# Kernel tuning notes

Measured on AMD Instinct MI355X. Metric: run time of the kernel, lower is better.

## Reference

```python
import jax, jax.numpy as jnp
import numpy as np

N_NODES = 50000
N_EDGES = 800000
HIDDEN = 128
IN_DIM = 128
OUT_DIM = 40
N_LAYERS = 3


def setup_inputs() -> dict:
    key = jax.random.key(0)
    ks = jax.random.split(key, 8)
    s = 1.0 / np.sqrt(HIDDEN)
    return {
        "x": jax.random.normal(ks[0], (N_NODES, IN_DIM), jnp.float32),
        "edge_index": jax.random.randint(ks[1], (2, N_EDGES), 0, N_NODES, jnp.int32),
        "W_in": jax.random.normal(ks[2], (IN_DIM, HIDDEN), jnp.float32) * s,
        "b_in": jnp.zeros((HIDDEN,), jnp.float32),
        "Wl": jax.random.normal(ks[3], (N_LAYERS, HIDDEN, HIDDEN), jnp.float32) * s,
        "Wr": jax.random.normal(ks[4], (N_LAYERS, HIDDEN, HIDDEN), jnp.float32) * s,
        "bl": jnp.zeros((N_LAYERS, HIDDEN), jnp.float32),
        "Wc1": jax.random.normal(ks[5], (HIDDEN, HIDDEN), jnp.float32) * s,
        "bc1": jnp.zeros((HIDDEN,), jnp.float32),
        "Wc2": jax.random.normal(ks[6], (HIDDEN, OUT_DIM), jnp.float32) * s,
        "bc2": jnp.zeros((OUT_DIM,), jnp.float32),
    }


def reference(x, edge_index, W_in, b_in, Wl, Wr, bl, Wc1, bc1, Wc2, bc2):
    src, dst = edge_index[0], edge_index[1]
    n = x.shape[0]
    # in-degree for mean aggregation (clamped to 1 for isolated nodes)
    deg = jax.ops.segment_sum(jnp.ones_like(src, x.dtype), dst, num_segments=n)
    deg_inv = (1.0 / jnp.maximum(deg, 1.0))[:, None]  # [N,1]

    h = x @ W_in + b_in  # lin1; dropout is identity in eval mode
    js = []
    for i in range(N_LAYERS):
        # GraphSAGE-mean: gather neighbor feats, scatter-mean, self + neighbor linear
        agg = jax.ops.segment_sum(h[src], dst, num_segments=n) * deg_inv
        h = jax.nn.relu(h @ Wl[i] + agg @ Wr[i] + bl[i])
        js.append(h)  # skip ops are identity; fix_last appends last layer directly

    x5 = js[0] + js[1] + js[2]  # layer aggregator 'l_sum' with linear activation
    hc = jax.nn.relu(x5 @ Wc1 + bc1)
    return hc @ Wc2 + bc2  # logits [N, OUT_DIM]
```

## Files before the change

kernel.cpp:

```cpp
#include <hip/hip_runtime.h>
#include <hip/hip_fp8.h>

#define NN   50000
#define NE   800000
#define HID  128
#define OUTD 40
#define NBLK 196
#define LIN_BLKS ((NN + 127) / 128)
#define DEG_BLKS ((NE + 255) / 256)

typedef float f32x4  __attribute__((ext_vector_type(4)));
typedef int   i32x4  __attribute__((ext_vector_type(4)));
typedef short bf16x8 __attribute__((ext_vector_type(8)));

__device__ __forceinline__ f32x4 mfma(bf16x8 a, bf16x8 b, f32x4 c) {
  return __builtin_amdgcn_mfma_f32_16x16x32_bf16(a, b, c, 0, 0, 0);
}
__device__ __forceinline__ unsigned short f2bf(float f) {
  unsigned u = __builtin_bit_cast(unsigned, f);
  u += 0x7fffu + ((u >> 16) & 1u);
  return (unsigned short)(u >> 16);
}
__device__ __forceinline__ unsigned pack2(float lo, float hi) {
  return (unsigned)f2bf(lo) | ((unsigned)f2bf(hi) << 16);
}
__device__ __forceinline__ float bflo(unsigned v){ return __builtin_bit_cast(float, v << 16); }
__device__ __forceinline__ float bfhi(unsigned v){ return __builtin_bit_cast(float, v & 0xffff0000u); }
__device__ __forceinline__ unsigned char f2fp8(float f) {
  return (unsigned char)__hip_fp8_e4m3(f).__x;
}
__device__ __forceinline__ void accfp8(float* a, uint4 v) {
  unsigned u[4] = {v.x, v.y, v.z, v.w};
#pragma unroll
  for (int i = 0; i < 4; i++) {
#pragma unroll
    for (int b = 0; b < 4; b++) {
      __hip_fp8_e4m3 t;
      t.__x = (__hip_fp8_storage_t)((u[i] >> (8 * b)) & 0xffu);
      a[i * 4 + b] += (float)t;
    }
  }
}

__global__ void k_blocksum(const int* __restrict__ deg, int* __restrict__ bsum) {
  __shared__ int s[256];
  int t = threadIdx.x, i = blockIdx.x * 256 + t;
  s[t] = (i < NN) ? deg[i] : 0;
  __syncthreads();
  for (int o = 128; o > 0; o >>= 1) { if (t < o) s[t] += s[t + o]; __syncthreads(); }
  if (t == 0) bsum[blockIdx.x] = s[0];
}

__global__ void k_scan3(const int* __restrict__ deg, const int* __restrict__ bsum,
                        int* __restrict__ offs, float* __restrict__ dinv) {
  __shared__ int sb[256];
  __shared__ int s[256];
  int t = threadIdx.x, i = blockIdx.x * 256 + t;
  sb[t] = (t < NBLK && t < blockIdx.x) ? bsum[t] : 0;
  int v = (i < NN) ? deg[i] : 0;
  s[t] = v;
  __syncthreads();
  for (int o = 128; o > 0; o >>= 1) { if (t < o) sb[t] += sb[t + o]; __syncthreads(); }
  for (int o = 1; o < 256; o <<= 1) {
    int x = (t >= o) ? s[t - o] : 0;
    __syncthreads(); s[t] += x; __syncthreads();
  }
  int off = sb[0] + s[t] - v;
  if (i < NN) {
    offs[i] = off;
    dinv[i] = 1.0f / (float)(v > 0 ? v : 1);
  }
  if (i == 0) offs[NN] = NE;
}

__global__ void k_fill(const int* __restrict__ src, const int* __restrict__ dst,
                       const int* __restrict__ pos, const int* __restrict__ offs,
                       int* __restrict__ csr) {
  int i = blockIdx.x * blockDim.x + threadIdx.x;
  if (i < NE) {
    csr[offs[dst[i]] + pos[i]] = src[i];
  }
}

__global__ void k_prep(const float* __restrict__ Win, const float* __restrict__ Wl,
                       const float* __restrict__ Wr, const float* __restrict__ Wc1,
                       const float* __restrict__ Wc2, unsigned short* __restrict__ wt,
                       int* __restrict__ deg) {
  int idx = blockIdx.x * 256 + threadIdx.x;
  if (idx < NN) deg[idx] = 0;
  const int NMAIN = 8 * 16384;
  if (idx >= NMAIN + 48 * 128) return;
  float v;
  if (idx < NMAIN) {
    int m = idx >> 14, rem = idx & 16383;
    int n = rem >> 7, k = rem & 127;
    const float* s;
    if (m == 0) s = Win;
    else if (m <= 3) s = Wl + (m - 1) * 16384;
    else if (m <= 6) s = Wr + (m - 4) * 16384;
    else s = Wc1;
    v = s[k * 128 + n];
  } else {
    int rem = idx - NMAIN;
    int n = rem >> 7, k = rem & 127;
    v = (n < OUTD) ? Wc2[k * OUTD + n] : 0.f;
  }
  wt[idx] = f2bf(v);
}

__device__ __forceinline__ void lin_in_body(int bid, const float* __restrict__ x,
                                            const unsigned short* __restrict__ Wt,
                                            const float* __restrict__ bias,
                                            unsigned short* __restrict__ hout,
                                            unsigned char* __restrict__ h8out) {
  const int lane = threadIdx.x & 63, w = threadIdx.x >> 6;
  const int wr = w >> 1, wc = w & 1;
  const int r15 = lane & 15, khi = lane >> 4;
  const int mbase = bid * 128 + wr * 64, nbase = wc * 64;
  f32x4 acc[4][4] = {};
#pragma unroll
  for (int ks = 0; ks < 4; ++ks) {
    const int kk = ks * 32 + khi * 8;
    bf16x8 af[4], bq[4];
#pragma unroll
    for (int i = 0; i < 4; i++) {
      int row = mbase + i * 16 + r15; row = row < NN ? row : NN - 1;
      const f32x4* p = (const f32x4*)(x + row * HID + kk);
      f32x4 lo = p[0], hi = p[1];
      i32x4 t;
      t[0] = pack2(lo[0], lo[1]); t[1] = pack2(lo[2], lo[3]);
      t[2] = pack2(hi[0], hi[1]); t[3] = pack2(hi[2], hi[3]);
      af[i] = __builtin_bit_cast(bf16x8, t);
    }
#pragma unroll
    for (int j = 0; j < 4; j++) {
      int col = nbase + j * 16 + r15;
      bq[j] = *(const bf16x8*)(Wt + col * HID + kk);
    }
#pragma unroll
    for (int i = 0; i < 4; i++)
#pragma unroll
      for (int j = 0; j < 4; j++) acc[i][j] = mfma(af[i], bq[j], acc[i][j]);
  }
  float b4[4];
#pragma unroll
  for (int j = 0; j < 4; j++) b4[j] = bias[nbase + j * 16 + r15];
#pragma unroll
  for (int i = 0; i < 4; i++) {
    const int rb = mbase + i * 16 + khi * 4;
#pragma unroll
    for (int e = 0; e < 4; e++) {
      const int r = rb + e;
      if (r < NN) {
#pragma unroll
        for (int j = 0; j < 4; j++) {
          float v = acc[i][j][e] + b4[j];
          const int col = nbase + j * 16 + r15;
          hout[r * HID + col] = f2bf(v);
          h8out[r * HID + col] = f2fp8(v);
        }
      }
    }
  }
}

__global__ __launch_bounds__(256) void k_deg_lin(const int* __restrict__ dst,
                                                 int* __restrict__ deg,
                                                 int* __restrict__ pos,
                                                 const float* __restrict__ x,
                                                 const unsigned short* __restrict__ Wt,
                                                 const float* __restrict__ bias,
                                                 unsigned short* __restrict__ hout,
                                                 unsigned char* __restrict__ h8out) {
  if (blockIdx.x < LIN_BLKS) {
    lin_in_body(blockIdx.x, x, Wt, bias, hout, h8out);
  } else {
    int i = (blockIdx.x - LIN_BLKS) * 256 + threadIdx.x;
    if (i < NE) pos[i] = atomicAdd(&deg[dst[i]], 1);
  }
}

__global__ __launch_bounds__(256) void k_agg(const unsigned char* __restrict__ h8,
                                             const int* __restrict__ csr,
                                             const int* __restrict__ offs,
                                             const float* __restrict__ dinv,
                                             unsigned short* __restrict__ agg) {
  const int lane = threadIdx.x & 63;
  const int c8 = lane & 7;
  const int o8 = lane >> 3;
  int gw = (blockIdx.x * 256 + (int)threadIdx.x) >> 6;
  const int nw = (gridDim.x * 256) >> 6;
  const uint4* h4 = (const uint4*)h8;
  uint4* ag4 = (uint4*)agg;
  for (int n = gw; n < NN; n += nw) {
    const int s = offs[n], e = offs[n + 1];
    float a[16];
#pragma unroll
    for (int j = 0; j < 16; j++) a[j] = 0.f;
    int k = s;
    int ia = 0, ib = 0;
    bool have = (k + 16 <= e);
    if (have) { ia = csr[k + o8]; ib = csr[k + 8 + o8]; }
    while (have) {
      uint4 va = h4[ia * 8 + c8];
      uint4 vb = h4[ib * 8 + c8];
      k += 16;
      have = (k + 16 <= e);
      if (have) { ia = csr[k + o8]; ib = csr[k + 8 + o8]; }
      accfp8(a, va);
      accfp8(a, vb);
    }
    for (; k < e; k += 8) {
      if (k + o8 < e) {
        uint4 v = h4[csr[k + o8] * 8 + c8];
        accfp8(a, v);
      }
    }
#pragma unroll
    for (int j = 0; j < 16; j++) {
      a[j] += __shfl_xor(a[j], 8);
      a[j] += __shfl_xor(a[j], 16);
      a[j] += __shfl_xor(a[j], 32);
    }
    if (o8 == 0) {
      float di = dinv[n];
      uint4 o0, o1;
      o0.x = pack2(a[0] * di, a[1] * di);
      o0.y = pack2(a[2] * di, a[3] * di);
      o0.z = pack2(a[4] * di, a[5] * di);
      o0.w = pack2(a[6] * di, a[7] * di);
      o1.x = pack2(a[8] * di, a[9] * di);
      o1.y = pack2(a[10] * di, a[11] * di);
      o1.z = pack2(a[12] * di, a[13] * di);
      o1.w = pack2(a[14] * di, a[15] * di);
      ag4[n * 16 + c8 * 2 + 0] = o0;
      ag4[n * 16 + c8 * 2 + 1] = o1;
    }
  }
}

__global__ __launch_bounds__(256) void k_layer(const unsigned short* __restrict__ hp,
                                               const unsigned short* __restrict__ ag,
                                               const unsigned short* __restrict__ WtL,
                                               const unsigned short* __restrict__ WtR,
                                               const float* __restrict__ bias,
                                               unsigned short* __restrict__ hout,
                                               unsigned char* __restrict__ h8out) {
  const int lane = threadIdx.x & 63, w = threadIdx.x >> 6;
  const int wr = w >> 1, wc = w & 1;
  const int r15 = lane & 15, khi = lane >> 4;
  const int mbase = blockIdx.x * 128 + wr * 64, nbase = wc * 64;
  f32x4 acc[4][4] = {};
#pragma unroll
  for (int ph = 0; ph < 2; ++ph) {
    const unsigned short* A = ph ? ag : hp;
    const unsigned short* B = ph ? WtR : WtL;
#pragma unroll
    for (int ks = 0; ks < 4; ++ks) {
      const int kk = ks * 32 + khi * 8;
      bf16x8 af[4], bq[4];
#pragma unroll
      for (int i = 0; i < 4; i++) {
        int row = mbase + i * 16 + r15; row = row < NN ? row : NN - 1;
        af[i] = *(const bf16x8*)(A + row * HID + kk);
      }
#pragma unroll
      for (int j = 0; j < 4; j++) {
        int col = nbase + j * 16 + r15;
        bq[j] = *(const bf16x8*)(B + col * HID + kk);
      }
#pragma unroll
      for (int i = 0; i < 4; i++)
#pragma unroll
        for (int j = 0; j < 4; j++) acc[i][j] = mfma(af[i], bq[j], acc[i][j]);
    }
  }
  float b4[4];
#pragma unroll
  for (int j = 0; j < 4; j++) b4[j] = bias[nbase + j * 16 + r15];
#pragma unroll
  for (int i = 0; i < 4; i++) {
    const int rb = mbase + i * 16 + khi * 4;
#pragma unroll
    for (int e = 0; e < 4; e++) {
      const int r = rb + e;
      if (r < NN) {
#pragma unroll
        for (int j = 0; j < 4; j++) {
          float v = acc[i][j][e] + b4[j];
          v = fmaxf(v, 0.f);
          const int col = nbase + j * 16 + r15;
          hout[r * HID + col] = f2bf(v);
          h8out[r * HID + col] = f2fp8(v);
        }
      }
    }
  }
}

__global__ __launch_bounds__(256) void k_cls(const unsigned short* __restrict__ h1,
                                             const unsigned short* __restrict__ h2,
                                             const unsigned short* __restrict__ h3,
                                             const unsigned short* __restrict__ WtC1,
                                             const float* __restrict__ bc1,
                                             const unsigned short* __restrict__ WtC2,
                                             const float* __restrict__ bc2,
                                             float* __restrict__ out) {
  __shared__ unsigned short hc[128 * 136];
  const int lane = threadIdx.x & 63, w = threadIdx.x >> 6;
  const int wr = w >> 1, wc = w & 1;
  const int r15 = lane & 15, khi = lane >> 4;
  const int mbase = blockIdx.x * 128 + wr * 64, nbase = wc * 64;
  {
    f32x4 acc[4][4] = {};
#pragma unroll
    for (int ks = 0; ks < 4; ++ks) {
      const int kk = ks * 32 + khi * 8;
      bf16x8 af[4], bq[4];
#pragma unroll
      for (int i = 0; i < 4; i++) {
        int row = mbase + i * 16 + r15; row = row < NN ? row : NN - 1;
        i32x4 u = *(const i32x4*)(h1 + row * HID + kk);
        i32x4 v = *(const i32x4*)(h2 + row * HID + kk);
        i32x4 q = *(const i32x4*)(h3 + row * HID + kk);
        i32x4 t;
#pragma unroll
        for (int cc = 0; cc < 4; cc++) {
          unsigned uu = u[cc], vv = v[cc], qq = q[cc];
          t[cc] = pack2(bflo(uu) + bflo(vv) + bflo(qq), bfhi(uu) + bfhi(vv) + bfhi(qq));
        }
        af[i] = __builtin_bit_cast(bf16x8, t);
      }
#pragma unroll
      for (int j = 0; j < 4; j++) {
        int col = nbase + j * 16 + r15;
        bq[j] = *(const bf16x8*)(WtC1 + col * HID + kk);
      }
#pragma unroll
      for (int i = 0; i < 4; i++)
#pragma unroll
        for (int j = 0; j < 4; j++) acc[i][j] = mfma(af[i], bq[j], acc[i][j]);
    }
    float b4[4];
#pragma unroll
    for (int j = 0; j < 4; j++) b4[j] = bc1[nbase + j * 16 + r15];
#pragma unroll
    for (int i = 0; i < 4; i++) {
      const int rT = wr * 64 + i * 16 + khi * 4;
#pragma unroll
      for (int e = 0; e < 4; e++) {
#pragma unroll
        for (int j = 0; j < 4; j++) {
          float v = fmaxf(acc[i][j][e] + b4[j], 0.f);
          hc[(rT + e) * 136 + nbase + j * 16 + r15] = f2bf(v);
        }
      }
    }
  }
  __syncthreads();
  {
    f32x4 a2[2][3] = {};
#pragma unroll
    for (int ks = 0; ks < 4; ++ks) {
      const int kk = ks * 32 + khi * 8;
      bf16x8 af[2], bq[3];
#pragma unroll
      for (int i = 0; i < 2; i++) {
        int rT = w * 32 + i * 16 + r15;
        af[i] = *(const bf16x8*)&hc[rT * 136 + kk];
      }
#pragma unroll
      for (int j = 0; j < 3; j++) {
        int col = j * 16 + r15;
        bq[j] = *(const bf16x8*)(WtC2 + col * HID + kk);
      }
#pragma unroll
      for (int i = 0; i < 2; i++)
#pragma unroll
        for (int j = 0; j < 3; j++) a2[i][j] = mfma(af[i], bq[j], a2[i][j]);
    }
#pragma unroll
    for (int j = 0; j < 3; j++) {
      const int col = j * 16 + r15;
      const float b = (col < OUTD) ? bc2[col] : 0.f;
#pragma unroll
      for (int i = 0; i < 2; i++) {
        const int rT = w * 32 + i * 16 + khi * 4;
#pragma unroll
        for (int e = 0; e < 4; e++) {
          const int gr = blockIdx.x * 128 + rT + e;
          if (gr < NN && col < OUTD) out[gr * OUTD + col] = a2[i][j][e] + b;
        }
      }
    }
  }
}

extern "C" void kernel_launch(void* const* d_in, const int* in_sizes, int n_in,
                              void* d_out, int out_size, void* d_ws, size_t ws_size,
                              hipStream_t stream) {
  (void)in_sizes; (void)n_in; (void)out_size; (void)ws_size;
  const float* x   = (const float*)d_in[0];
  const int*   ei  = (const int*)d_in[1];
  const float* Win = (const float*)d_in[2];
  const float* bin = (const float*)d_in[3];
  const float* Wl  = (const float*)d_in[4];
  const float* Wr  = (const float*)d_in[5];
  const float* bl  = (const float*)d_in[6];
  const float* Wc1 = (const float*)d_in[7];
  const float* bc1 = (const float*)d_in[8];
  const float* Wc2 = (const float*)d_in[9];
  const float* bc2 = (const float*)d_in[10];
  float* out = (float*)d_out;

  char* ws = (char*)d_ws;
  size_t off = 0;
  auto take = [&](size_t bytes) -> char* {
    char* p = ws + off; off = (off + bytes + 255) & ~(size_t)255; return p;
  };
  int* deg        = (int*)take((size_t)NN * 4);
  int* offs       = (int*)take((size_t)(NN + 1) * 4);
  int* pos        = (int*)take((size_t)NE * 4);
  int* bsum       = (int*)take(256 * 4);
  float* dinv     = (float*)take((size_t)NN * 4);
  int* csr        = (int*)take((size_t)NE * 4);
  unsigned short* wt  = (unsigned short*)take((size_t)(8 * 16384 + 48 * 128) * 2);
  unsigned short* h0  = (unsigned short*)take((size_t)NN * HID * 2);
  unsigned short* h1  = (unsigned short*)take((size_t)NN * HID * 2);
  unsigned short* h2  = (unsigned short*)take((size_t)NN * HID * 2);
  unsigned short* h3  = (unsigned short*)take((size_t)NN * HID * 2);
  unsigned short* agg = (unsigned short*)take((size_t)NN * HID * 2);
  unsigned char* h8_0 = (unsigned char*)take((size_t)NN * HID);
  unsigned char* h8_1 = (unsigned char*)take((size_t)NN * HID);
  unsigned char* h8_2 = (unsigned char*)take((size_t)NN * HID);

  const int* esrc = ei;
  const int* edst = ei + NE;

  k_prep<<<(8 * 16384 + 48 * 128 + 255) / 256, 256, 0, stream>>>(Win, Wl, Wr, Wc1, Wc2, wt, deg);
  k_deg_lin<<<LIN_BLKS + DEG_BLKS, 256, 0, stream>>>(edst, deg, pos, x, wt, bin, h0, h8_0);
  k_blocksum<<<NBLK, 256, 0, stream>>>(deg, bsum);
  k_scan3<<<NBLK, 256, 0, stream>>>(deg, bsum, offs, dinv);
  k_fill<<<(NE + 255) / 256, 256, 0, stream>>>(esrc, edst, pos, offs, csr);

  unsigned short* hs[4] = {h0, h1, h2, h3};
  unsigned char* h8s[3] = {h8_0, h8_1, h8_2};
  for (int i = 0; i < 3; i++) {
    k_agg<<<2048, 256, 0, stream>>>(h8s[i], csr, offs, dinv, agg);
    unsigned char* h8next = (i < 2) ? h8s[i + 1] : h8_0;
    k_layer<<<(NN + 127) / 128, 256, 0, stream>>>(hs[i], agg, wt + (1 + i) * 16384,
                                                  wt + (4 + i) * 16384, bl + i * HID,
                                                  hs[i + 1], h8next);
  }
  k_cls<<<(NN + 127) / 128, 256, 0, stream>>>(h1, h2, h3, wt + 7 * 16384, bc1,
                                              wt + 8 * 16384, bc2, out);
}
```

Baseline: 276.1 us.

## Replicate degree counters to cut atomic contention and use hardware fp8 converts

```diff
diff --git a/kernel.cpp b/kernel.cpp
--- a/kernel.cpp
+++ b/kernel.cpp
@@ -1,5 +1,4 @@
 #include <hip/hip_runtime.h>
-#include <hip/hip_fp8.h>
 
 #define NN   50000
 #define NE   800000
@@ -8,8 +7,10 @@
 #define NBLK 196
 #define LIN_BLKS ((NN + 127) / 128)
 #define DEG_BLKS ((NE + 255) / 256)
+#define NREP 8
 
 typedef float f32x4  __attribute__((ext_vector_type(4)));
+typedef float f32x2  __attribute__((ext_vector_type(2)));
 typedef int   i32x4  __attribute__((ext_vector_type(4)));
 typedef short bf16x8 __attribute__((ext_vector_type(8)));
 
@@ -27,37 +28,47 @@
 __device__ __forceinline__ float bflo(unsigned v){ return __builtin_bit_cast(float, v << 16); }
 __device__ __forceinline__ float bfhi(unsigned v){ return __builtin_bit_cast(float, v & 0xffff0000u); }
 __device__ __forceinline__ unsigned char f2fp8(float f) {
-  return (unsigned char)__hip_fp8_e4m3(f).__x;
+  int p = __builtin_amdgcn_cvt_pk_fp8_f32(f, f, 0, false);
+  return (unsigned char)(p & 0xff);
 }
 __device__ __forceinline__ void accfp8(float* a, uint4 v) {
   unsigned u[4] = {v.x, v.y, v.z, v.w};
 #pragma unroll
   for (int i = 0; i < 4; i++) {
-#pragma unroll
-    for (int b = 0; b < 4; b++) {
-      __hip_fp8_e4m3 t;
-      t.__x = (__hip_fp8_storage_t)((u[i] >> (8 * b)) & 0xffu);
-      a[i * 4 + b] += (float)t;
-    }
-  }
-}
-
-__global__ void k_blocksum(const int* __restrict__ deg, int* __restrict__ bsum) {
+    f32x2 lo = __builtin_amdgcn_cvt_pk_f32_fp8((int)u[i], false);
+    f32x2 hi = __builtin_amdgcn_cvt_pk_f32_fp8((int)u[i], true);
+    a[i * 4 + 0] += lo[0]; a[i * 4 + 1] += lo[1];
+    a[i * 4 + 2] += hi[0]; a[i * 4 + 3] += hi[1];
+  }
+}
+
+__global__ void k_blocksum(const int* __restrict__ deg8, int* __restrict__ bsum) {
   __shared__ int s[256];
   int t = threadIdx.x, i = blockIdx.x * 256 + t;
-  s[t] = (i < NN) ? deg[i] : 0;
+  int d = 0;
+  if (i < NN) {
+#pragma unroll
+    for (int r = 0; r < NREP; r++) d += deg8[r * NN + i];
+  }
+  s[t] = d;
   __syncthreads();
   for (int o = 128; o > 0; o >>= 1) { if (t < o) s[t] += s[t + o]; __syncthreads(); }
   if (t == 0) bsum[blockIdx.x] = s[0];
 }
 
-__global__ void k_scan3(const int* __restrict__ deg, const int* __restrict__ bsum,
-                        int* __restrict__ offs, float* __restrict__ dinv) {
+__global__ void k_scan3(const int* __restrict__ deg8, const int* __restrict__ bsum,
+                        int* __restrict__ offs, float* __restrict__ dinv,
+                        int* __restrict__ abs8) {
   __shared__ int sb[256];
   __shared__ int s[256];
   int t = threadIdx.x, i = blockIdx.x * 256 + t;
   sb[t] = (t < NBLK && t < blockIdx.x) ? bsum[t] : 0;
-  int v = (i < NN) ? deg[i] : 0;
+  int dr[NREP];
+  int v = 0;
+  if (i < NN) {
+#pragma unroll
+    for (int r = 0; r < NREP; r++) { dr[r] = deg8[r * NN + i]; v += dr[r]; }
+  }
   s[t] = v;
   __syncthreads();
   for (int o = 128; o > 0; o >>= 1) { if (t < o) sb[t] += sb[t + o]; __syncthreads(); }
@@ -69,25 +80,30 @@
   if (i < NN) {
     offs[i] = off;
     dinv[i] = 1.0f / (float)(v > 0 ? v : 1);
+    int running = off;
+#pragma unroll
+    for (int r = 0; r < NREP; r++) { abs8[r * NN + i] = running; running += dr[r]; }
   }
   if (i == 0) offs[NN] = NE;
 }
 
 __global__ void k_fill(const int* __restrict__ src, const int* __restrict__ dst,
-                       const int* __restrict__ pos, const int* __restrict__ offs,
+                       const int* __restrict__ pos, const int* __restrict__ abs8,
                        int* __restrict__ csr) {
   int i = blockIdx.x * blockDim.x + threadIdx.x;
   if (i < NE) {
-    csr[offs[dst[i]] + pos[i]] = src[i];
+    int r = i & (NREP - 1);
+    csr[abs8[r * NN + dst[i]] + pos[i]] = src[i];
   }
 }
 
 __global__ void k_prep(const float* __restrict__ Win, const float* __restrict__ Wl,
                        const float* __restrict__ Wr, const float* __restrict__ Wc1,
                        const float* __restrict__ Wc2, unsigned short* __restrict__ wt,
-                       int* __restrict__ deg) {
+                       int* __restrict__ deg8) {
   int idx = blockIdx.x * 256 + threadIdx.x;
-  if (idx < NN) deg[idx] = 0;
+  const int NT = ((8 * 16384 + 48 * 128 + 255) / 256) * 256;
+  for (int j = idx; j < NREP * NN; j += NT) deg8[j] = 0;
   const int NMAIN = 8 * 16384;
   if (idx >= NMAIN + 48 * 128) return;
   float v;
@@ -165,7 +181,7 @@
 }
 
 __global__ __launch_bounds__(256) void k_deg_lin(const int* __restrict__ dst,
-                                                 int* __restrict__ deg,
+                                                 int* __restrict__ deg8,
                                                  int* __restrict__ pos,
                                                  const float* __restrict__ x,
                                                  const unsigned short* __restrict__ Wt,
@@ -176,7 +192,10 @@
     lin_in_body(blockIdx.x, x, Wt, bias, hout, h8out);
   } else {
     int i = (blockIdx.x - LIN_BLKS) * 256 + threadIdx.x;
-    if (i < NE) pos[i] = atomicAdd(&deg[dst[i]], 1);
+    if (i < NE) {
+      int r = i & (NREP - 1);
+      pos[i] = atomicAdd(&deg8[r * NN + dst[i]], 1);
+    }
   }
 }
 
@@ -418,7 +437,8 @@
   auto take = [&](size_t bytes) -> char* {
     char* p = ws + off; off = (off + bytes + 255) & ~(size_t)255; return p;
   };
-  int* deg        = (int*)take((size_t)NN * 4);
+  int* deg8       = (int*)take((size_t)NREP * NN * 4);
+  int* abs8       = (int*)take((size_t)NREP * NN * 4);
   int* offs       = (int*)take((size_t)(NN + 1) * 4);
   int* pos        = (int*)take((size_t)NE * 4);
   int* bsum       = (int*)take(256 * 4);
@@ -437,11 +457,11 @@
   const int* esrc = ei;
   const int* edst = ei + NE;
 
-  k_prep<<<(8 * 16384 + 48 * 128 + 255) / 256, 256, 0, stream>>>(Win, Wl, Wr, Wc1, Wc2, wt, deg);
-  k_deg_lin<<<LIN_BLKS + DEG_BLKS, 256, 0, stream>>>(edst, deg, pos, x, wt, bin, h0, h8_0);
-  k_blocksum<<<NBLK, 256, 0, stream>>>(deg, bsum);
-  k_scan3<<<NBLK, 256, 0, stream>>>(deg, bsum, offs, dinv);
-  k_fill<<<(NE + 255) / 256, 256, 0, stream>>>(esrc, edst, pos, offs, csr);
+  k_prep<<<(8 * 16384 + 48 * 128 + 255) / 256, 256, 0, stream>>>(Win, Wl, Wr, Wc1, Wc2, wt, deg8);
+  k_deg_lin<<<LIN_BLKS + DEG_BLKS, 256, 0, stream>>>(edst, deg8, pos, x, wt, bin, h0, h8_0);
+  k_blocksum<<<NBLK, 256, 0, stream>>>(deg8, bsum);
+  k_scan3<<<NBLK, 256, 0, stream>>>(deg8, bsum, offs, dinv, abs8);
+  k_fill<<<(NE + 255) / 256, 256, 0, stream>>>(esrc, edst, pos, abs8, csr);
 
   unsigned short* hs[4] = {h0, h1, h2, h3};
   unsigned char* h8s[3] = {h8_0, h8_1, h8_2};
```

Result: faster. 269.9 us (-2.2%).
